# Kernel tuning notes

Measured on AMD Instinct MI355X. Metric: run time of the kernel, lower is better.

## Reference

```python
import jax, jax.numpy as jnp
import numpy as np

C = 512
CD = C // 8  # query/key channel dim
EPS = 1e-5


def conv1x1(x, W, b):
    # x: [B,C,H,W], W: [Cout,Cin], b: [Cout]
    return jnp.einsum('bchw,dc->bdhw', x, W) + b[None, :, None, None]


def criss_cross(x, Wq, bq, Wk, bk, Wv, bv, gamma):
    B, Cc, H, Wd = x.shape
    q = conv1x1(x, Wq, bq)   # [B,CD,H,W]
    k = conv1x1(x, Wk, bk)   # [B,CD,H,W]
    v = conv1x1(x, Wv, bv)   # [B,C,H,W]
    # column (height) path energies: e_H[b,h,w,g] = <q[:, :,h,w], k[:,:,g,w]>
    e_h = jnp.einsum('bdhw,bdgw->bhwg', q, k)
    diag = jnp.eye(H, dtype=bool)[:, None, :]          # [H,1,H] over (h,g)
    e_h = jnp.where(diag[None], -jnp.inf, e_h)          # -inf on self position (CCNet INF mask)
    # row (width) path energies: e_w[b,h,w,v] = <q[:,:,h,w], k[:,:,h,v]>
    e_w = jnp.einsum('bdhw,bdhv->bhwv', q, k)
    att = jax.nn.softmax(jnp.concatenate([e_h, e_w], axis=-1), axis=-1)  # [B,H,W,H+W]
    a_h, a_w = att[..., :H], att[..., H:]
    out_h = jnp.einsum('bhwg,bcgw->bchw', a_h, v)
    out_w = jnp.einsum('bhwv,bchv->bchw', a_w, v)
    return gamma * (out_h + out_w) + x


def batchnorm2d(x, w, b):
    mean = jnp.mean(x, axis=(0, 2, 3), keepdims=True)
    var = jnp.var(x, axis=(0, 2, 3), keepdims=True)  # biased variance (training-mode BN)
    return (x - mean) * jax.lax.rsqrt(var + EPS) * w[None, :, None, None] + b[None, :, None, None]


def setup_inputs() -> dict:
    key = jax.random.key(0)
    ks = jax.random.split(key, 9)
    B, H, W = 8, 96, 96
    s_in = 1.0 / np.sqrt(C)
    return {
        'x': jax.random.normal(ks[0], (B, C, H, W), dtype=jnp.float32),
        'Wq': jax.random.normal(ks[1], (CD, C), dtype=jnp.float32) * s_in,
        'bq': jax.random.normal(ks[2], (CD,), dtype=jnp.float32) * 0.01,
        'Wk': jax.random.normal(ks[3], (CD, C), dtype=jnp.float32) * s_in,
        'bk': jax.random.normal(ks[4], (CD,), dtype=jnp.float32) * 0.01,
        'Wv': jax.random.normal(ks[5], (C, C), dtype=jnp.float32) * s_in,
        'bv': jax.random.normal(ks[6], (C,), dtype=jnp.float32) * 0.01,
        'gamma': jnp.float32(0.5),
        'bn_weight': jnp.ones((C,), dtype=jnp.float32) + 0.1 * jax.random.normal(ks[7], (C,), dtype=jnp.float32),
        'bn_bias': 0.1 * jax.random.normal(ks[8], (C,), dtype=jnp.float32),
        'recurrent': 2,
    }


def reference(x, Wq, bq, Wk, bk, Wv, bv, gamma, bn_weight, bn_bias, recurrent):
    for _ in range(recurrent):
        x = criss_cross(x, Wq, bq, Wk, bk, Wv, bv, gamma)
    return batchnorm2d(x, bn_weight, bn_bias)
```

## Files before the change

kernel.cpp:

```cpp
#include <hip/hip_runtime.h>
#include <math.h>


typedef short s16x8 __attribute__((ext_vector_type(8)));
typedef short s16x4 __attribute__((ext_vector_type(4)));
typedef float f32x4 __attribute__((ext_vector_type(4)));
typedef unsigned short us;

namespace {
constexpr int kB = 8;
constexpr int kC = 512;
constexpr int kH = 96;
constexpr int kW = 96;
constexpr int kHW = kH * kW;
constexpr int kN = kB * kHW;
}

__device__ inline us f2bf(float f) {
  union { float f; unsigned u; } v;
  v.f = f;
  const unsigned r = v.u + 0x7fffu + ((v.u >> 16) & 1u);
  return (us)(r >> 16);
}
__device__ inline float bf2f(us h) {
  union { unsigned u; float f; } v;
  v.u = ((unsigned)h) << 16;
  return v.f;
}

__global__ __launch_bounds__(256) void k_tr_in(const float* __restrict__ in,
                                               us* __restrict__ outb,
                                               us* __restrict__ outlo) {
  __shared__ float tile[64][33];
  const int b = blockIdx.z;
  const int n0 = blockIdx.x * 32;
  const int c0 = blockIdx.y * 64;
  const int tx = threadIdx.x;
  const int ty = threadIdx.y;
#pragma unroll
  for (int i = 0; i < 8; ++i) {
    const int c = c0 + ty + 8 * i;
    tile[ty + 8 * i][tx] = in[((size_t)b * kC + c) * kHW + n0 + tx];
  }
  __syncthreads();
#pragma unroll
  for (int i = 0; i < 4; ++i) {
    const int n = n0 + ty + 8 * i;
    const float f0 = tile[2 * tx][ty + 8 * i];
    const float f1 = tile[2 * tx + 1][ty + 8 * i];
    const us h0 = f2bf(f0), h1 = f2bf(f1);
    const size_t o = ((size_t)b * kHW + n) * kC + c0 + 2 * tx;
    *(unsigned*)&outb[o] = (unsigned)h0 | ((unsigned)h1 << 16);
    *(unsigned*)&outlo[o] =
        (unsigned)f2bf(f0 - bf2f(h0)) | ((unsigned)f2bf(f1 - bf2f(h1)) << 16);
  }
}

__global__ __launch_bounds__(256) void k_cvt_wqk(const float* __restrict__ Wq,
                                                 const float* __restrict__ Wk,
                                                 us* __restrict__ whi,
                                                 us* __restrict__ wlo) {
  const int i = blockIdx.x * 256 + threadIdx.x;
  const int m = i >> 9, c = i & 511;
  const float v = m < 64 ? Wq[m * kC + c] : Wk[(m - 64) * kC + c];
  const us hi = f2bf(v);
  whi[i] = hi;
  wlo[i] = f2bf(v - bf2f(hi));
}
__global__ __launch_bounds__(256) void k_cvt_wv(const float* __restrict__ Wv,
                                                us* __restrict__ wvb) {
  const int i = blockIdx.x * 256 + threadIdx.x;
  wvb[i] = f2bf(Wv[i]);
}

__global__ __launch_bounds__(256) void k_gemm_qk(
    const us* __restrict__ xtb, const us* __restrict__ xtlo,
    const us* __restrict__ whi, const us* __restrict__ wlo,
    const float* __restrict__ bq, const float* __restrict__ bk,
    float* __restrict__ qk) {
  __shared__ __align__(16) us AsH[128 * 64];
  __shared__ __align__(16) us AsL[128 * 64];
  __shared__ __align__(16) us BsH[128 * 64];
  __shared__ __align__(16) us BsL[128 * 64];
  const int bid = blockIdx.x;
  const int n0 = ((bid & 7) * 72 + (bid >> 3)) * 128;
  const int tid = threadIdx.x, lane = tid & 63;
  const int wr = (tid >> 6) >> 1, wc = (tid >> 6) & 1;
  const int l15 = lane & 15, kg = lane >> 4;
  f32x4 acc[4][4] = {};
  for (int kk = 0; kk < kC; kk += 64) {
    __syncthreads();
#pragma unroll
    for (int p = 0; p < 4; ++p) {
      const int idx = p * 256 + tid;
      const int r = idx >> 3, c8 = idx & 7;
      const int cs = (c8 ^ (r & 7)) * 8;
      const int db = (p * 256 + (tid & 192)) * 8;
      const size_t ga = (size_t)(n0 + r) * kC + kk + cs;
      const size_t gb = (size_t)r * kC + kk + cs;
      __builtin_amdgcn_global_load_lds((const unsigned*)&xtb[ga],
                                       (unsigned*)&AsH[db], 16, 0, 0);
      __builtin_amdgcn_global_load_lds((const unsigned*)&xtlo[ga],
                                       (unsigned*)&AsL[db], 16, 0, 0);
      __builtin_amdgcn_global_load_lds((const unsigned*)&whi[gb],
                                       (unsigned*)&BsH[db], 16, 0, 0);
      __builtin_amdgcn_global_load_lds((const unsigned*)&wlo[gb],
                                       (unsigned*)&BsL[db], 16, 0, 0);
    }
    __syncthreads();
#pragma unroll
    for (int ks = 0; ks < 2; ++ks) {
      s16x8 ah[4], al[4], bh[4], bl[4];
#pragma unroll
      for (int mf = 0; mf < 4; ++mf) {
        const int r = wr * 64 + mf * 16 + l15;
        const int off = r * 64 + (((ks * 4 + kg) ^ (r & 7)) << 3);
        ah[mf] = *(const s16x8*)&AsH[off];
        al[mf] = *(const s16x8*)&AsL[off];
      }
#pragma unroll
      for (int nf = 0; nf < 4; ++nf) {
        const int r = wc * 64 + nf * 16 + l15;
        const int off = r * 64 + (((ks * 4 + kg) ^ (r & 7)) << 3);
        bh[nf] = *(const s16x8*)&BsH[off];
        bl[nf] = *(const s16x8*)&BsL[off];
      }
#pragma unroll
      for (int nf = 0; nf < 4; ++nf)
#pragma unroll
        for (int mf = 0; mf < 4; ++mf) {
          acc[nf][mf] = __builtin_amdgcn_mfma_f32_16x16x32_bf16(
              bh[nf], ah[mf], acc[nf][mf], 0, 0, 0);
          acc[nf][mf] = __builtin_amdgcn_mfma_f32_16x16x32_bf16(
              bh[nf], al[mf], acc[nf][mf], 0, 0, 0);
          acc[nf][mf] = __builtin_amdgcn_mfma_f32_16x16x32_bf16(
              bl[nf], ah[mf], acc[nf][mf], 0, 0, 0);
        }
    }
  }
#pragma unroll
  for (int nf = 0; nf < 4; ++nf) {
    const int mq = wc * 64 + nf * 16 + kg * 4;
    const f32x4 b4 = *(const f32x4*)((wc == 0) ? &bq[mq] : &bk[mq - 64]);
#pragma unroll
    for (int mf = 0; mf < 4; ++mf) {
      const int n = n0 + wr * 64 + mf * 16 + l15;
      *(f32x4*)&qk[(size_t)n * 128 + mq] = acc[nf][mf] + b4;
    }
  }
}

__global__ __launch_bounds__(256) void k_att_col(const float* __restrict__ qk,
                                                 const us* __restrict__ xtb,
                                                 us* __restrict__ aggxb,
                                                 float2* __restrict__ ms) {
  __shared__ __align__(16) char smem[2 * 96 * 65 * 4];
  __shared__ __align__(16) us Ps[96 * 104];
  float* Qs = (float*)smem;
  float* Ks = Qs + 96 * 65;
  us* Xs = (us*)smem;
  const int w = blockIdx.x;
  const int b = blockIdx.y;
  const int tid = threadIdx.x;
  const size_t qkbase = ((size_t)b * kHW + w) * 128;
  for (int idx = tid; idx < 96 * 32; idx += 256) {
    const int h = idx >> 5, m4 = (idx & 31) * 4;
    const float4 v = *(const float4*)&qk[qkbase + (size_t)h * (kW * 128) + m4];
    float* dst = (m4 < 64) ? &Qs[h * 65 + m4] : &Ks[h * 65 + m4 - 64];
    dst[0] = v.x; dst[1] = v.y; dst[2] = v.z; dst[3] = v.w;
  }
  __syncthreads();
  const int tx = tid & 15, ty = tid >> 4;
  float E[6][6];
#pragma unroll
  for (int i = 0; i < 6; ++i)
#pragma unroll
    for (int j = 0; j < 6; ++j) E[i][j] = 0.f;
  for (int dd = 0; dd < 64; ++dd) {
    float qr[6], kr[6];
#pragma unroll
    for (int i = 0; i < 6; ++i) qr[i] = Qs[(ty + 16 * i) * 65 + dd];
#pragma unroll
    for (int j = 0; j < 6; ++j) kr[j] = Ks[(tx + 16 * j) * 65 + dd];
#pragma unroll
    for (int i = 0; i < 6; ++i)
#pragma unroll
      for (int j = 0; j < 6; ++j) E[i][j] += qr[i] * kr[j];
  }
#pragma unroll
  for (int i = 0; i < 6; ++i) {
    if (tx == ty) E[i][i] = -1e30f;
    const int row = ty + 16 * i;
    float mx = E[i][0];
#pragma unroll
    for (int j = 1; j < 6; ++j) mx = fmaxf(mx, E[i][j]);
#pragma unroll
    for (int off = 1; off < 16; off <<= 1) mx = fmaxf(mx, __shfl_xor(mx, off, 64));
    float sm = 0.f;
#pragma unroll
    for (int j = 0; j < 6; ++j) {
      const float e = __expf(E[i][j] - mx);
      sm += e;
      Ps[row * 104 + tx + 16 * j] = f2bf(e);
    }
#pragma unroll
    for (int off = 1; off < 16; off <<= 1) sm += __shfl_xor(sm, off, 64);
    if (tx == 0) ms[(size_t)b * kHW + (size_t)row * kW + w] = make_float2(mx, sm);
  }
  __syncthreads();
  const int lane = tid & 63, wave = tid >> 6, l15 = lane & 15, kg = lane >> 4;
  for (int c0 = 0; c0 < kC; c0 += 128) {
    for (int idx = tid; idx < 96 * 16; idx += 256) {
      const int g = idx >> 4, c8 = idx & 15;
      const s16x8 v = *(const s16x8*)
          &xtb[((size_t)b * kHW + (size_t)g * kW + w) * kC + c0 + c8 * 8];
#pragma unroll
      for (int i2 = 0; i2 < 8; ++i2) Xs[(c8 * 8 + i2) * 104 + g] = v[i2];
    }
    __syncthreads();
    f32x4 acc[2][6] = {};
#pragma unroll
    for (int ks = 0; ks < 3; ++ks) {
      s16x8 xf[2], pf[6];
#pragma unroll
      for (int nf = 0; nf < 2; ++nf)
        xf[nf] = *(const s16x8*)
            &Xs[((wave * 2 + nf) * 16 + l15) * 104 + ks * 32 + kg * 8];
#pragma unroll
      for (int mf = 0; mf < 6; ++mf)
        pf[mf] = *(const s16x8*)&Ps[(mf * 16 + l15) * 104 + ks * 32 + kg * 8];
#pragma unroll
      for (int nf = 0; nf < 2; ++nf)
#pragma unroll
        for (int mf = 0; mf < 6; ++mf)
          acc[nf][mf] = __builtin_amdgcn_mfma_f32_16x16x32_bf16(
              xf[nf], pf[mf], acc[nf][mf], 0, 0, 0);
    }
#pragma unroll
    for (int mf = 0; mf < 6; ++mf) {
      const int h = mf * 16 + l15;
      const size_t rb = ((size_t)b * kHW + (size_t)h * kW + w) * kC;
#pragma unroll
      for (int nf = 0; nf < 2; ++nf) {
        const int c = c0 + (wave * 2 + nf) * 16 + kg * 4;
        s16x4 st;
#pragma unroll
        for (int i = 0; i < 4; ++i) st[i] = (short)f2bf(acc[nf][mf][i]);
        *(s16x4*)&aggxb[rb + c] = st;
      }
    }
    __syncthreads();
  }
}

__global__ __launch_bounds__(256) void k_att_row(const float* __restrict__ qk,
                                                 const us* __restrict__ xtb,
                                                 us* __restrict__ aggxb,
                                                 const float2* __restrict__ ms) {
  __shared__ __align__(16) char smem[2 * 96 * 65 * 4];
  __shared__ __align__(16) us Ps[96 * 104];
  __shared__ float2 al[96];
  float* Qs = (float*)smem;
  float* Ks = Qs + 96 * 65;
  us* Xs = (us*)smem;
  const int h = blockIdx.x;
  const int b = blockIdx.y;
  const int tid = threadIdx.x;
  const size_t qkbase = ((size_t)b * kHW + (size_t)h * kW) * 128;
  for (int idx = tid; idx < 96 * 32; idx += 256) {
    const int v = idx >> 5, m4 = (idx & 31) * 4;
    const float4 q4 = *(const float4*)&qk[qkbase + (size_t)v * 128 + m4];
    float* dst = (m4 < 64) ? &Qs[v * 65 + m4] : &Ks[v * 65 + m4 - 64];
    dst[0] = q4.x; dst[1] = q4.y; dst[2] = q4.z; dst[3] = q4.w;
  }
  __syncthreads();
  const int tx = tid & 15, ty = tid >> 4;
  float E[6][6];
#pragma unroll
  for (int i = 0; i < 6; ++i)
#pragma unroll
    for (int j = 0; j < 6; ++j) E[i][j] = 0.f;
  for (int dd = 0; dd < 64; ++dd) {
    float qr[6], kr[6];
#pragma unroll
    for (int i = 0; i < 6; ++i) qr[i] = Qs[(ty + 16 * i) * 65 + dd];
#pragma unroll
    for (int j = 0; j < 6; ++j) kr[j] = Ks[(tx + 16 * j) * 65 + dd];
#pragma unroll
    for (int i = 0; i < 6; ++i)
#pragma unroll
      for (int j = 0; j < 6; ++j) E[i][j] += qr[i] * kr[j];
  }
#pragma unroll
  for (int i = 0; i < 6; ++i) {
    const int row = ty + 16 * i;
    float mx = E[i][0];
#pragma unroll
    for (int j = 1; j < 6; ++j) mx = fmaxf(mx, E[i][j]);
#pragma unroll
    for (int off = 1; off < 16; off <<= 1) mx = fmaxf(mx, __shfl_xor(mx, off, 64));
    float sm = 0.f;
#pragma unroll
    for (int j = 0; j < 6; ++j) {
      const float e = __expf(E[i][j] - mx);
      sm += e;
      Ps[row * 104 + tx + 16 * j] = f2bf(e);
    }
#pragma unroll
    for (int off = 1; off < 16; off <<= 1) sm += __shfl_xor(sm, off, 64);
    if (tx == 0) {
      const float2 mh = ms[(size_t)b * kHW + (size_t)h * kW + row];
      const float M = fmaxf(mh.x, mx);
      const float eh = __expf(mh.x - M), ew = __expf(mx - M);
      const float S = mh.y * eh + sm * ew;
      al[row] = make_float2(eh / S, ew / S);
    }
  }
  __syncthreads();
  const int lane = tid & 63, wave = tid >> 6, l15 = lane & 15, kg = lane >> 4;
  for (int c0 = 0; c0 < kC; c0 += 128) {
    for (int idx = tid; idx < 96 * 16; idx += 256) {
      const int v = idx >> 4, c8 = idx & 15;
      const s16x8 x8 = *(const s16x8*)
          &xtb[((size_t)b * kHW + (size_t)h * kW + v) * kC + c0 + c8 * 8];
#pragma unroll
      for (int i2 = 0; i2 < 8; ++i2) Xs[(c8 * 8 + i2) * 104 + v] = x8[i2];
    }
    __syncthreads();
    f32x4 acc[2][6] = {};
#pragma unroll
    for (int ks = 0; ks < 3; ++ks) {
      s16x8 xf[2], pf[6];
#pragma unroll
      for (int nf = 0; nf < 2; ++nf)
        xf[nf] = *(const s16x8*)
            &Xs[((wave * 2 + nf) * 16 + l15) * 104 + ks * 32 + kg * 8];
#pragma unroll
      for (int mf = 0; mf < 6; ++mf)
        pf[mf] = *(const s16x8*)&Ps[(mf * 16 + l15) * 104 + ks * 32 + kg * 8];
#pragma unroll
      for (int nf = 0; nf < 2; ++nf)
#pragma unroll
        for (int mf = 0; mf < 6; ++mf)
          acc[nf][mf] = __builtin_amdgcn_mfma_f32_16x16x32_bf16(
              xf[nf], pf[mf], acc[nf][mf], 0, 0, 0);
    }
#pragma unroll
    for (int mf = 0; mf < 6; ++mf) {
      const int w = mf * 16 + l15;
      const float2 a2 = al[w];
      const size_t rb = ((size_t)b * kHW + (size_t)h * kW + w) * kC;
#pragma unroll
      for (int nf = 0; nf < 2; ++nf) {
        const int c = c0 + (wave * 2 + nf) * 16 + kg * 4;
        const s16x4 old = *(const s16x4*)&aggxb[rb + c];
        s16x4 st;
#pragma unroll
        for (int i = 0; i < 4; ++i)
          st[i] = (short)f2bf(a2.x * bf2f((us)old[i]) + a2.y * acc[nf][mf][i]);
        *(s16x4*)&aggxb[rb + c] = st;
      }
    }
    __syncthreads();
  }
}

template <bool LAST>
__global__ __launch_bounds__(256) void k_proj_mfma(
    const us* __restrict__ aggxb, const us* __restrict__ wvb,
    const float* __restrict__ bv, const float* __restrict__ gammap,
    us* __restrict__ xtb, us* __restrict__ xtlo, float* __restrict__ stats) {
  __shared__ __align__(16) us As[128 * 64];
  __shared__ __align__(16) us Bs[128 * 64];
  __shared__ float bnS[128], bnQ[128];
  const int flat = blockIdx.x;
  const int swz = (flat & 7) * 288 + (flat >> 3);
  const int n0 = (swz >> 2) * 128;
  const int m0 = (swz & 3) * 128;
  const int tid = threadIdx.x, lane = tid & 63;
  const int wr = (tid >> 6) >> 1, wc = (tid >> 6) & 1;
  const int l15 = lane & 15, kg = lane >> 4;
  if (LAST && tid < 128) { bnS[tid] = 0.f; bnQ[tid] = 0.f; }
  f32x4 acc[4][4] = {};
  for (int kk = 0; kk < kC; kk += 64) {
    __syncthreads();
#pragma unroll
    for (int p = 0; p < 4; ++p) {
      const int idx = p * 256 + tid;
      const int r = idx >> 3, c8 = idx & 7;
      const int cs = (c8 ^ (r & 7)) * 8;
      const int db = (p * 256 + (tid & 192)) * 8;
      __builtin_amdgcn_global_load_lds(
          (const unsigned*)&aggxb[(size_t)(n0 + r) * kC + kk + cs],
          (unsigned*)&As[db], 16, 0, 0);
      __builtin_amdgcn_global_load_lds(
          (const unsigned*)&wvb[(size_t)(m0 + r) * kC + kk + cs],
          (unsigned*)&Bs[db], 16, 0, 0);
    }
    __syncthreads();
#pragma unroll
    for (int ks = 0; ks < 2; ++ks) {
      s16x8 a[4], b[4];
#pragma unroll
      for (int mf = 0; mf < 4; ++mf) {
        const int r = wr * 64 + mf * 16 + l15;
        a[mf] = *(const s16x8*)&As[r * 64 + (((ks * 4 + kg) ^ (r & 7)) << 3)];
      }
#pragma unroll
      for (int nf = 0; nf < 4; ++nf) {
        const int r = wc * 64 + nf * 16 + l15;
        b[nf] = *(const s16x8*)&Bs[r * 64 + (((ks * 4 + kg) ^ (r & 7)) << 3)];
      }
#pragma unroll
      for (int nf = 0; nf < 4; ++nf)
#pragma unroll
        for (int mf = 0; mf < 4; ++mf)
          acc[nf][mf] = __builtin_amdgcn_mfma_f32_16x16x32_bf16(
              b[nf], a[mf], acc[nf][mf], 0, 0, 0);
    }
  }
  const float g = gammap[0];
  float ps_[4][4], pq_[4][4];
  if (LAST) {
#pragma unroll
    for (int nf = 0; nf < 4; ++nf)
#pragma unroll
      for (int i = 0; i < 4; ++i) { ps_[nf][i] = 0.f; pq_[nf][i] = 0.f; }
  }
#pragma unroll
  for (int mf = 0; mf < 4; ++mf) {
    const int n = n0 + wr * 64 + mf * 16 + l15;
#pragma unroll
    for (int nf = 0; nf < 4; ++nf) {
      const int mq = m0 + wc * 64 + nf * 16 + kg * 4;
      const size_t o = (size_t)n * kC + mq;
      const f32x4 b4 = *(const f32x4*)&bv[mq];
      const s16x4 uh = *(const s16x4*)&xtb[o];
      const s16x4 ul = *(const s16x4*)&xtlo[o];
      s16x4 nh, nl;
#pragma unroll
      for (int i = 0; i < 4; ++i) {
        const float x = bf2f((us)uh[i]) + bf2f((us)ul[i]);
        const float r = g * (acc[nf][mf][i] + b4[i]) + x;
        const us hi = f2bf(r);
        nh[i] = (short)hi;
        nl[i] = (short)f2bf(r - bf2f(hi));
        if (LAST) { ps_[nf][i] += r; pq_[nf][i] += r * r; }
      }
      *(s16x4*)&xtb[o] = nh;
      *(s16x4*)&xtlo[o] = nl;
    }
  }
  if (LAST) {
#pragma unroll
    for (int nf = 0; nf < 4; ++nf)
#pragma unroll
      for (int i = 0; i < 4; ++i) {
        float s = ps_[nf][i], q = pq_[nf][i];
#pragma unroll
        for (int off = 1; off < 16; off <<= 1) {
          s += __shfl_xor(s, off, 64);
          q += __shfl_xor(q, off, 64);
        }
        if (l15 == 0) {
          const int cl = wc * 64 + nf * 16 + kg * 4 + i;
          atomicAdd(&bnS[cl], s);
          atomicAdd(&bnQ[cl], q);
        }
      }
    __syncthreads();
    if (tid < 128) {
      atomicAdd(&stats[m0 + tid], bnS[tid]);
      atomicAdd(&stats[kC + m0 + tid], bnQ[tid]);
    }
  }
}

__global__ __launch_bounds__(256) void k_bn_apply(
    const us* __restrict__ xtb, const us* __restrict__ xtlo,
    const float* __restrict__ stats, const float* __restrict__ bw,
    const float* __restrict__ bb, float* __restrict__ out) {
  __shared__ float tile[64][33];
  __shared__ float sc[64], sh[64];
  const int b = blockIdx.z;
  const int n0 = blockIdx.x * 32;
  const int c0 = blockIdx.y * 64;
  const int tx = threadIdx.x;
  const int ty = threadIdx.y;
  const int tid = ty * 32 + tx;
  if (tid < 64) {
    const int c = c0 + tid;
    const float mean = stats[c] * (1.f / (float)kN);
    const float var = stats[kC + c] * (1.f / (float)kN) - mean * mean;
    const float r = rsqrtf(var + 1e-5f);
    sc[tid] = r * bw[c];
    sh[tid] = bb[c] - mean * r * bw[c];
  }
  __syncthreads();
#pragma unroll
  for (int i = 0; i < 4; ++i) {
    const int n = n0 + ty + 8 * i;
    const size_t o = ((size_t)b * kHW + n) * kC + c0 + 2 * tx;
    const unsigned uh = *(const unsigned*)&xtb[o];
    const unsigned ul = *(const unsigned*)&xtlo[o];
    const float v0 = bf2f((us)uh) + bf2f((us)ul);
    const float v1 = bf2f((us)(uh >> 16)) + bf2f((us)(ul >> 16));
    tile[2 * tx][ty + 8 * i] = v0 * sc[2 * tx] + sh[2 * tx];
    tile[2 * tx + 1][ty + 8 * i] = v1 * sc[2 * tx + 1] + sh[2 * tx + 1];
  }
  __syncthreads();
#pragma unroll
  for (int i = 0; i < 8; ++i) {
    const int cc = ty + 8 * i;
    out[((size_t)b * kC + c0 + cc) * kHW + n0 + tx] = tile[cc][tx];
  }
}

extern "C" void kernel_launch(void* const* d_in, const int* in_sizes, int n_in,
                              void* d_out, int out_size, void* d_ws,
                              size_t ws_size, hipStream_t stream) {
  const float* x_in = (const float*)d_in[0];
  const float* Wq = (const float*)d_in[1];
  const float* bq = (const float*)d_in[2];
  const float* Wk = (const float*)d_in[3];
  const float* bk = (const float*)d_in[4];
  const float* Wv = (const float*)d_in[5];
  const float* bv = (const float*)d_in[6];
  const float* gamma = (const float*)d_in[7];
  const float* bnw = (const float*)d_in[8];
  const float* bnb = (const float*)d_in[9];

  constexpr size_t NC = (size_t)kN * kC;
  us* xtb = (us*)d_ws;
  us* xtlo = xtb + NC;
  float* qk = (float*)(xtlo + NC);
  us* aggxb = (us*)(qk + (size_t)kN * 128);
  float2* ms = (float2*)(aggxb + NC);
  us* wqkhi = (us*)(ms + kN);
  us* wqklo = wqkhi + 128 * kC;
  us* wvb = wqklo + 128 * kC;
  float* stats = (float*)(wvb + kC * kC);

  k_tr_in<<<dim3(kHW / 32, kC / 64, kB), dim3(32, 8), 0, stream>>>(x_in, xtb,
                                                                   xtlo);
  k_cvt_wqk<<<dim3(128 * kC / 256), 256, 0, stream>>>(Wq, Wk, wqkhi, wqklo);
  k_cvt_wv<<<dim3(kC * kC / 256), 256, 0, stream>>>(Wv, wvb);
  hipMemsetAsync(stats, 0, 1024 * sizeof(float), stream);

  for (int it = 0; it < 2; ++it) {
    k_gemm_qk<<<dim3(kN / 128), 256, 0, stream>>>(xtb, xtlo, wqkhi, wqklo, bq,
                                                  bk, qk);
    k_att_col<<<dim3(kW, kB), 256, 0, stream>>>(qk, xtb, aggxb, ms);
    k_att_row<<<dim3(kH, kB), 256, 0, stream>>>(qk, xtb, aggxb, ms);
    if (it == 0)
      k_proj_mfma<false><<<dim3((kN / 128) * 4), 256, 0, stream>>>(
          aggxb, wvb, bv, gamma, xtb, xtlo, stats);
    else
      k_proj_mfma<true><<<dim3((kN / 128) * 4), 256, 0, stream>>>(
          aggxb, wvb, bv, gamma, xtb, xtlo, stats);
  }

  k_bn_apply<<<dim3(kHW / 32, kC / 64, kB), dim3(32, 8), 0, stream>>>(
      xtb, xtlo, stats, bnw, bnb, (float*)d_out);
}
```

Measured before the change: 796.1 us.

## Prefetch X tiles in registers for attention and double-buffer projection GEMM LDS

In the column and row attention kernels, the first 128-channel X slice is loaded into registers at kernel start, before the QK energy computation. Each later slice is fetched while the current slice is being used, so global load latency overlaps with compute. The value-projection GEMM now double-buffers its A/B LDS tiles, issuing async global-to-LDS loads for the next K step while MFMAs run on the current one, with one barrier per iteration. This raises register and LDS use, which may lower occupancy.

```diff
diff --git a/kernel.cpp b/kernel.cpp
--- a/kernel.cpp
+++ b/kernel.cpp
@@ -162,6 +162,14 @@
   const int w = blockIdx.x;
   const int b = blockIdx.y;
   const int tid = threadIdx.x;
+  s16x8 xr[6];
+#pragma unroll
+  for (int u = 0; u < 6; ++u) {
+    const int idx = tid + 256 * u;
+    const int g = idx >> 4, c8 = idx & 15;
+    xr[u] = *(const s16x8*)
+        &xtb[((size_t)b * kHW + (size_t)g * kW + w) * kC + c8 * 8];
+  }
   const size_t qkbase = ((size_t)b * kHW + w) * 128;
   for (int idx = tid; idx < 96 * 32; idx += 256) {
     const int h = idx >> 5, m4 = (idx & 31) * 4;
@@ -209,13 +217,23 @@
   }
   __syncthreads();
   const int lane = tid & 63, wave = tid >> 6, l15 = lane & 15, kg = lane >> 4;
-  for (int c0 = 0; c0 < kC; c0 += 128) {
-    for (int idx = tid; idx < 96 * 16; idx += 256) {
+  for (int cc = 0; cc < 4; ++cc) {
+    const int c0 = cc * 128;
+#pragma unroll
+    for (int u = 0; u < 6; ++u) {
+      const int idx = tid + 256 * u;
       const int g = idx >> 4, c8 = idx & 15;
-      const s16x8 v = *(const s16x8*)
-          &xtb[((size_t)b * kHW + (size_t)g * kW + w) * kC + c0 + c8 * 8];
-#pragma unroll
-      for (int i2 = 0; i2 < 8; ++i2) Xs[(c8 * 8 + i2) * 104 + g] = v[i2];
+#pragma unroll
+      for (int i2 = 0; i2 < 8; ++i2) Xs[(c8 * 8 + i2) * 104 + g] = xr[u][i2];
+    }
+    if (cc < 3) {
+#pragma unroll
+      for (int u = 0; u < 6; ++u) {
+        const int idx = tid + 256 * u;
+        const int g = idx >> 4, c8 = idx & 15;
+        xr[u] = *(const s16x8*)
+            &xtb[((size_t)b * kHW + (size_t)g * kW + w) * kC + c0 + 128 + c8 * 8];
+      }
     }
     __syncthreads();
     f32x4 acc[2][6] = {};
@@ -266,6 +284,14 @@
   const int h = blockIdx.x;
   const int b = blockIdx.y;
   const int tid = threadIdx.x;
+  s16x8 xr[6];
+#pragma unroll
+  for (int u = 0; u < 6; ++u) {
+    const int idx = tid + 256 * u;
+    const int v = idx >> 4, c8 = idx & 15;
+    xr[u] = *(const s16x8*)
+        &xtb[((size_t)b * kHW + (size_t)h * kW + v) * kC + c8 * 8];
+  }
   const size_t qkbase = ((size_t)b * kHW + (size_t)h * kW) * 128;
   for (int idx = tid; idx < 96 * 32; idx += 256) {
     const int v = idx >> 5, m4 = (idx & 31) * 4;
@@ -318,13 +344,23 @@
   }
   __syncthreads();
   const int lane = tid & 63, wave = tid >> 6, l15 = lane & 15, kg = lane >> 4;
-  for (int c0 = 0; c0 < kC; c0 += 128) {
-    for (int idx = tid; idx < 96 * 16; idx += 256) {
+  for (int cc = 0; cc < 4; ++cc) {
+    const int c0 = cc * 128;
+#pragma unroll
+    for (int u = 0; u < 6; ++u) {
+      const int idx = tid + 256 * u;
       const int v = idx >> 4, c8 = idx & 15;
-      const s16x8 x8 = *(const s16x8*)
-          &xtb[((size_t)b * kHW + (size_t)h * kW + v) * kC + c0 + c8 * 8];
-#pragma unroll
-      for (int i2 = 0; i2 < 8; ++i2) Xs[(c8 * 8 + i2) * 104 + v] = x8[i2];
+#pragma unroll
+      for (int i2 = 0; i2 < 8; ++i2) Xs[(c8 * 8 + i2) * 104 + v] = xr[u][i2];
+    }
+    if (cc < 3) {
+#pragma unroll
+      for (int u = 0; u < 6; ++u) {
+        const int idx = tid + 256 * u;
+        const int v = idx >> 4, c8 = idx & 15;
+        xr[u] = *(const s16x8*)
+            &xtb[((size_t)b * kHW + (size_t)h * kW + v) * kC + c0 + 128 + c8 * 8];
+      }
     }
     __syncthreads();
     f32x4 acc[2][6] = {};
@@ -370,8 +406,8 @@
     const us* __restrict__ aggxb, const us* __restrict__ wvb,
     const float* __restrict__ bv, const float* __restrict__ gammap,
     us* __restrict__ xtb, us* __restrict__ xtlo, float* __restrict__ stats) {
-  __shared__ __align__(16) us As[128 * 64];
-  __shared__ __align__(16) us Bs[128 * 64];
+  __shared__ __align__(16) us As[2][128 * 64];
+  __shared__ __align__(16) us Bs[2][128 * 64];
   __shared__ float bnS[128], bnQ[128];
   const int flat = blockIdx.x;
   const int swz = (flat & 7) * 288 + (flat >> 3);
@@ -381,9 +417,8 @@
   const int wr = (tid >> 6) >> 1, wc = (tid >> 6) & 1;
   const int l15 = lane & 15, kg = lane >> 4;
   if (LAST && tid < 128) { bnS[tid] = 0.f; bnQ[tid] = 0.f; }
-  f32x4 acc[4][4] = {};
-  for (int kk = 0; kk < kC; kk += 64) {
-    __syncthreads();
+
+  auto stage = [&](int buf, int kk) {
 #pragma unroll
     for (int p = 0; p < 4; ++p) {
       const int idx = p * 256 + tid;
@@ -392,24 +427,31 @@
       const int db = (p * 256 + (tid & 192)) * 8;
       __builtin_amdgcn_global_load_lds(
           (const unsigned*)&aggxb[(size_t)(n0 + r) * kC + kk + cs],
-          (unsigned*)&As[db], 16, 0, 0);
+          (unsigned*)&As[buf][db], 16, 0, 0);
       __builtin_amdgcn_global_load_lds(
           (const unsigned*)&wvb[(size_t)(m0 + r) * kC + kk + cs],
-          (unsigned*)&Bs[db], 16, 0, 0);
-    }
-    __syncthreads();
+          (unsigned*)&Bs[buf][db], 16, 0, 0);
+    }
+  };
+
+  f32x4 acc[4][4] = {};
+  stage(0, 0);
+  __syncthreads();
+  for (int t = 0; t < 8; ++t) {
+    const int cur = t & 1;
+    if (t < 7) stage(cur ^ 1, (t + 1) * 64);
 #pragma unroll
     for (int ks = 0; ks < 2; ++ks) {
       s16x8 a[4], b[4];
 #pragma unroll
       for (int mf = 0; mf < 4; ++mf) {
         const int r = wr * 64 + mf * 16 + l15;
-        a[mf] = *(const s16x8*)&As[r * 64 + (((ks * 4 + kg) ^ (r & 7)) << 3)];
+        a[mf] = *(const s16x8*)&As[cur][r * 64 + (((ks * 4 + kg) ^ (r & 7)) << 3)];
       }
 #pragma unroll
       for (int nf = 0; nf < 4; ++nf) {
         const int r = wc * 64 + nf * 16 + l15;
-        b[nf] = *(const s16x8*)&Bs[r * 64 + (((ks * 4 + kg) ^ (r & 7)) << 3)];
+        b[nf] = *(const s16x8*)&Bs[cur][r * 64 + (((ks * 4 + kg) ^ (r & 7)) << 3)];
       }
 #pragma unroll
       for (int nf = 0; nf < 4; ++nf)
@@ -418,6 +460,7 @@
           acc[nf][mf] = __builtin_amdgcn_mfma_f32_16x16x32_bf16(
               b[nf], a[mf], acc[nf][mf], 0, 0, 0);
     }
+    __syncthreads();
   }
   const float g = gammap[0];
   float ps_[4][4], pq_[4][4];
```

Result: no change. 804.8 us (+1.1%).
